# Kernel optimization log

Measured on AMD Instinct MI355X. Metric: run time of the kernel, lower is better.

## Reference

```python
import jax, jax.numpy as jnp
import numpy as np

B, L, D, H, HD, FF, NL = 2, 2048, 1024, 16, 64, 4096, 2
EPS = 1e-5
NEG = -1e30


def setup_inputs() -> dict:
    key = jax.random.key(0)
    ks = jax.random.split(key, 20)
    x = jax.random.normal(ks[0], (B, L, D), jnp.float32)
    # RoPE tables, rotate-half convention: [L, HD]
    pos = jnp.arange(L, dtype=jnp.float32)
    freqs = 1.0 / (10000.0 ** (jnp.arange(0, HD, 2, dtype=jnp.float32) / HD))
    ang = pos[:, None] * freqs[None, :]              # [L, HD/2]
    cos = jnp.concatenate([jnp.cos(ang), jnp.cos(ang)], -1)
    sin = jnp.concatenate([jnp.sin(ang), jnp.sin(ang)], -1)
    s = 0.02
    wq = jax.random.normal(ks[1], (NL, D, D), jnp.float32) * s
    wk = jax.random.normal(ks[2], (NL, D, D), jnp.float32) * s
    wv = jax.random.normal(ks[3], (NL, D, D), jnp.float32) * s
    wo = jax.random.normal(ks[4], (NL, D, D), jnp.float32) * s
    w1 = jax.random.normal(ks[5], (NL, D, FF), jnp.float32) * s
    w2 = jax.random.normal(ks[6], (NL, FF, D), jnp.float32) * s
    w3 = jax.random.normal(ks[7], (NL, D, FF), jnp.float32) * s
    attn_norm = jnp.ones((NL, D), jnp.float32)
    mlp_norm = jnp.ones((NL, D), jnp.float32)
    final_norm = jnp.ones((D,), jnp.float32)
    rw1 = jax.random.normal(ks[8], (D, D), jnp.float32) * s
    rb1 = jnp.zeros((D,), jnp.float32)
    rw2 = jax.random.normal(ks[9], (D, 1), jnp.float32) * s
    rb2 = jnp.zeros((1,), jnp.float32)
    return dict(x=x, cos=cos, sin=sin, wq=wq, wk=wk, wv=wv, wo=wo,
                w1=w1, w2=w2, w3=w3, attn_norm=attn_norm, mlp_norm=mlp_norm,
                final_norm=final_norm, rw1=rw1, rb1=rb1, rw2=rw2, rb2=rb2)


def _rms(x, w):
    return x * jax.lax.rsqrt(jnp.mean(x * x, -1, keepdims=True) + EPS) * w


def _rope(t, cos, sin):
    # t: [B, L, H, HD]; cos/sin: [L, HD]
    t1, t2 = jnp.split(t, 2, axis=-1)
    rot = jnp.concatenate([-t2, t1], -1)
    return t * cos[None, :, None, :] + rot * sin[None, :, None, :]


def reference(x, cos, sin, wq, wk, wv, wo, w1, w2, w3,
              attn_norm, mlp_norm, final_norm, rw1, rb1, rw2, rb2):
    causal = jnp.tril(jnp.ones((L, L), bool))
    h = x
    for i in range(NL):  # small fixed layer loop
        a = _rms(h, attn_norm[i])
        q = _rope((a @ wq[i]).reshape(B, L, H, HD), cos, sin)
        k = _rope((a @ wk[i]).reshape(B, L, H, HD), cos, sin)
        v = (a @ wv[i]).reshape(B, L, H, HD)
        sc = jnp.einsum('bqhd,bkhd->bhqk', q, k) / np.float32(np.sqrt(HD))
        sc = jnp.where(causal, sc, NEG)
        o = jnp.einsum('bhqk,bkhd->bqhd', jax.nn.softmax(sc, -1), v)
        h = h + o.reshape(B, L, D) @ wo[i]
        m = _rms(h, mlp_norm[i])
        h = h + (jax.nn.silu(m @ w1[i]) * (m @ w3[i])) @ w2[i]
    h = _rms(h, final_norm)

    # router chunking: straight-through hard boundaries
    logits = (jax.nn.silu(h @ rw1 + rb1) @ rw2 + rb2)[..., 0]   # [B, L]
    probs = jax.nn.sigmoid(logits)
    hard = (probs > 0.5).astype(h.dtype)
    mask = probs + jax.lax.stop_gradient(hard - probs)
    mask = mask.at[:, 0].set(1.0)
    mhard = jax.lax.stop_gradient(mask)
    # select matrix: S padded to static upper bound L (rows >= counts are zero)
    cums = jnp.cumsum(mhard, -1)                                # [B, L]
    seg = jnp.arange(1, L + 1, dtype=cums.dtype)[None, :, None] # [1, S, 1]
    assignment = (cums[:, None, :] == seg).astype(h.dtype)      # [B, S, L]
    select = assignment * mask[:, None, :]
    compressed = jnp.einsum('bsl,bld->bsd', select, h)          # [B, S, D]
    boundary_positions = jnp.argsort(-mhard, axis=-1)           # stable in jax
    counts = mhard.sum(-1).astype(jnp.int32)
    avg_chunk_size = jnp.float32(L) / jnp.mean(counts.astype(jnp.float32))
    return (h, compressed, boundary_positions, counts, avg_chunk_size)
```

## Files before the change

kernel.cpp:

```cpp
#include <hip/hip_runtime.h>
#include <cmath>

#define B_  2
#define L_  2048
#define D_  1024
#define H_  16
#define FF_ 4096
#define NL_ 2
#define NT_ (B_*L_)
#define ND_ (NT_*D_)

typedef __attribute__((ext_vector_type(8))) short bf16x8;
typedef __attribute__((ext_vector_type(4))) float f32x4;

__device__ __forceinline__ short f2bf(float x){
  unsigned u = __builtin_bit_cast(unsigned, x);
  unsigned r = (u + 0x7fffu + ((u>>16)&1u)) >> 16;
  return (short)r;
}
__device__ __forceinline__ float bf2f(short s){
  unsigned u = ((unsigned)(unsigned short)s) << 16;
  return __builtin_bit_cast(float, u);
}
#define MFMA16(a,b,c) __builtin_amdgcn_mfma_f32_16x16x32_bf16(a,b,c,0,0,0)

__device__ __forceinline__ void gload16(const short* g, short* l){
  __builtin_amdgcn_global_load_lds((const __attribute__((address_space(1))) void*)g,
                                   (__attribute__((address_space(3))) void*)l, 16, 0, 0);
}

template<bool WF32>
__global__ __launch_bounds__(256) void k_rmsnorm_s(const float* __restrict__ in,
                                                   const float* __restrict__ w,
                                                   short* __restrict__ oh,
                                                   short* __restrict__ ol,
                                                   float* __restrict__ of){
  int row = blockIdx.x; int tid = threadIdx.x;
  float4 xv = ((const float4*)(in + (size_t)row*D_))[tid];
  float ss = xv.x*xv.x + xv.y*xv.y + xv.z*xv.z + xv.w*xv.w;
  #pragma unroll
  for (int off=32; off; off>>=1) ss += __shfl_xor(ss, off);
  __shared__ float wsum[4];
  if ((tid&63)==0) wsum[tid>>6] = ss;
  __syncthreads();
  float tot = wsum[0]+wsum[1]+wsum[2]+wsum[3];
  float scale = 1.0f / sqrtf(tot*(1.0f/(float)D_) + 1e-5f);
  float4 w4 = ((const float4*)w)[tid];
  float v[4] = {xv.x*scale*w4.x, xv.y*scale*w4.y, xv.z*scale*w4.z, xv.w*scale*w4.w};
  short4 hh, ll;
  short h0=f2bf(v[0]); hh.x=h0; ll.x=f2bf(v[0]-bf2f(h0));
  short h1=f2bf(v[1]); hh.y=h1; ll.y=f2bf(v[1]-bf2f(h1));
  short h2=f2bf(v[2]); hh.z=h2; ll.z=f2bf(v[2]-bf2f(h2));
  short h3=f2bf(v[3]); hh.w=h3; ll.w=f2bf(v[3]-bf2f(h3));
  *(short4*)(oh + (size_t)row*D_ + tid*4) = hh;
  *(short4*)(ol + (size_t)row*D_ + tid*4) = ll;
  if (WF32){
    float4 ov; ov.x=v[0]; ov.y=v[1]; ov.z=v[2]; ov.w=v[3];
    ((float4*)(of + (size_t)row*D_))[tid] = ov;
  }
}

__global__ __launch_bounds__(256) void k_wsplit(const float* __restrict__ src,
                                                short* __restrict__ dh,
                                                short* __restrict__ dl,
                                                int srcN, int kOff, int nOff, int KT){
  __shared__ float t[64][68];
  int k0 = blockIdx.x*64, n0v = blockIdx.y*64;
  int tid = threadIdx.x;
  #pragma unroll
  for (int p=0;p<4;p++){
    int r = p*16 + (tid>>4);
    int c4 = (tid&15)*4;
    float4 v = *(const float4*)(src + (size_t)(kOff + k0 + r)*srcN + nOff + n0v + c4);
    *(float4*)&t[r][c4] = v;
  }
  __syncthreads();
  int n = tid>>2, kk = (tid&3)*16;
  bf16x8 H0, L0, H1, L1;
  #pragma unroll
  for (int q=0;q<8;q++){
    float v = t[kk+q][n]; short h=f2bf(v); H0[q]=h; L0[q]=f2bf(v-bf2f(h));
  }
  #pragma unroll
  for (int q=0;q<8;q++){
    float v = t[kk+8+q][n]; short h=f2bf(v); H1[q]=h; L1[q]=f2bf(v-bf2f(h));
  }
  size_t dof = (size_t)(n0v + n)*KT + k0 + kk;
  *(bf16x8*)(dh + dof) = H0;  *(bf16x8*)(dh + dof + 8) = H1;
  *(bf16x8*)(dl + dof) = L0;  *(bf16x8*)(dl + dof + 8) = L1;
}

__global__ __launch_bounds__(256,2) void k_qkv_mm(const short* __restrict__ Ah,
                                                  const short* __restrict__ Al,
                                                  const short* __restrict__ Wh,
                                                  const short* __restrict__ Wl,
                                                  short* __restrict__ OutH){
  __shared__ short lds[32768];
  int tid = threadIdx.x, wid = tid>>6, lane = tid&63;
  int l15 = lane&15, l4 = lane>>4;
  int wr = wid>>1, wc = wid&1;
  int m0 = blockIdx.y*128, n0 = blockIdx.x*128;
  const int K = 1024;
  f32x4 acc[4][4];
  #pragma unroll
  for (int i=0;i<4;i++){
    #pragma unroll
    for (int j=0;j<4;j++) acc[i][j] = (f32x4){0.f,0.f,0.f,0.f};
  }
  const short* gsrc = (wid==0)?Ah:(wid==1)?Al:(wid==2)?Wh:Wl;
  int rb = (wid<2)? m0 : n0;
  int gcol = ((lane&7)^(lane>>3))*8;
  short* ldsw = lds + wid*8192;
  const short* gp0 = gsrc + (size_t)(rb + (lane>>3))*K + gcol;
  for (int k0=0; k0<K; k0+=64){
    const short* gp = gp0 + k0;
    #pragma unroll
    for (int lc=0; lc<16; ++lc)
      gload16(gp + (size_t)lc*8*K, ldsw + lc*512);
    __syncthreads();
    #pragma unroll
    for (int ks=0; ks<2; ++ks){
      bf16x8 af[4], alf[4], wf[4], wlf[4];
      int gs = ((ks*4 + l4) ^ (lane&7))*8;
      #pragma unroll
      for (int f=0; f<4; ++f){
        int ar = (wr*64 + f*16 + l15)*64 + gs;
        af[f]  = *(const bf16x8*)&lds[ar];
        alf[f] = *(const bf16x8*)&lds[8192 + ar];
        int wr2 = (wc*64 + f*16 + l15)*64 + gs;
        wf[f]  = *(const bf16x8*)&lds[16384 + wr2];
        wlf[f] = *(const bf16x8*)&lds[24576 + wr2];
      }
      #pragma unroll
      for (int i=0;i<4;i++){
        #pragma unroll
        for (int j=0;j<4;j++){
          acc[i][j] = MFMA16(af[i],  wf[j],  acc[i][j]);
          acc[i][j] = MFMA16(alf[i], wf[j],  acc[i][j]);
          acc[i][j] = MFMA16(af[i],  wlf[j], acc[i][j]);
        }
      }
    }
    __syncthreads();
  }
  int sel = n0 >> 10;
  short* oh = OutH + (size_t)sel*8388608;
  short* ol = oh + 4194304;
  int cb = (n0 & 1023) + wc*64;
  #pragma unroll
  for (int i=0;i<4;i++){
    #pragma unroll
    for (int j=0;j<4;j++){
      #pragma unroll
      for (int r=0;r<4;r++){
        size_t mg = (size_t)(m0 + wr*64 + i*16 + l4*4 + r);
        int ng = cb + j*16 + l15;
        float v = acc[i][j][r];
        short h = f2bf(v);
        oh[mg*1024 + ng] = h;
        ol[mg*1024 + ng] = f2bf(v - bf2f(h));
      }
    }
  }
}

template<int EPI>
__global__ __launch_bounds__(256,2) void k_mm64(const short* __restrict__ Ah,
                                                const short* __restrict__ Al,
                                                const short* __restrict__ Wh,
                                                const short* __restrict__ Wl,
                                                const short* __restrict__ W3h,
                                                const short* __restrict__ W3l,
                                                int K,
                                                float* __restrict__ Cf,
                                                const float* __restrict__ bias,
                                                short* __restrict__ Gh,
                                                short* __restrict__ Gl,
                                                int ldc){
  __shared__ short lds[(EPI==3)?32768:24576];
  int tid = threadIdx.x, wid = tid>>6, lane = tid&63;
  int l15 = lane&15, l4 = lane>>4;
  int m0 = blockIdx.y*128, n0 = blockIdx.x*64;
  f32x4 a1[2][4], a3[2][4];
  #pragma unroll
  for (int i=0;i<2;i++){
    #pragma unroll
    for (int j=0;j<4;j++){ a1[i][j]=(f32x4){0.f,0.f,0.f,0.f}; a3[i][j]=(f32x4){0.f,0.f,0.f,0.f}; }
  }
  int gcol = ((lane&7)^(lane>>3))*8;
  int l8 = lane>>3;
  const int NCH = (EPI==3)? 16 : 12;
  for (int k0=0; k0<K; k0+=64){
    for (int t=0; t<NCH; ++t){
      int c = wid*NCH + t;
      const short* sb; int row0; short* db;
      if (c < 32){
        sb = (c<16)? Ah : Al; row0 = m0 + (c&15)*8;
        db = lds + ((c<16)?0:8192) + (c&15)*512;
      } else {
        int wseg = (c-32)>>3;
        sb = (wseg==0)?Wh:(wseg==1)?Wl:(wseg==2)?W3h:W3l;
        row0 = n0 + (c&7)*8;
        db = lds + 16384 + wseg*4096 + (c&7)*512;
      }
      gload16(sb + (size_t)(row0 + l8)*K + k0 + gcol, db);
    }
    __syncthreads();
    #pragma unroll
    for (int ks=0; ks<2; ++ks){
      int gs = ((ks*4 + l4) ^ (lane&7))*8;
      bf16x8 af[2], alf[2], wh[4], wl[4];
      #pragma unroll
      for (int f=0; f<2; ++f){
        int ar = (wid*32 + f*16 + l15)*64 + gs;
        af[f]  = *(const bf16x8*)&lds[ar];
        alf[f] = *(const bf16x8*)&lds[8192 + ar];
      }
      #pragma unroll
      for (int f=0; f<4; ++f){
        int wr2 = (f*16 + l15)*64 + gs;
        wh[f] = *(const bf16x8*)&lds[16384 + wr2];
        wl[f] = *(const bf16x8*)&lds[20480 + wr2];
      }
      #pragma unroll
      for (int i=0;i<2;i++){
        #pragma unroll
        for (int j=0;j<4;j++){
          a1[i][j] = MFMA16(af[i],  wh[j], a1[i][j]);
          a1[i][j] = MFMA16(alf[i], wh[j], a1[i][j]);
          a1[i][j] = MFMA16(af[i],  wl[j], a1[i][j]);
        }
      }
      if (EPI==3){
        bf16x8 w3h[4], w3l[4];
        #pragma unroll
        for (int f=0; f<4; ++f){
          int wr2 = (f*16 + l15)*64 + gs;
          w3h[f] = *(const bf16x8*)&lds[24576 + wr2];
          w3l[f] = *(const bf16x8*)&lds[28672 + wr2];
        }
        #pragma unroll
        for (int i=0;i<2;i++){
          #pragma unroll
          for (int j=0;j<4;j++){
            a3[i][j] = MFMA16(af[i],  w3h[j], a3[i][j]);
            a3[i][j] = MFMA16(alf[i], w3h[j], a3[i][j]);
            a3[i][j] = MFMA16(af[i],  w3l[j], a3[i][j]);
          }
        }
      }
    }
    __syncthreads();
  }
  #pragma unroll
  for (int i=0;i<2;i++){
    #pragma unroll
    for (int j=0;j<4;j++){
      #pragma unroll
      for (int r=0;r<4;r++){
        size_t mg = (size_t)(m0 + wid*32 + i*16 + l4*4 + r);
        int ng = n0 + j*16 + l15;
        float v = a1[i][j][r];
        if (EPI==1){
          float* cp = Cf + mg*ldc + ng;
          *cp = *cp + v;
        } else if (EPI==2){
          float x = v + bias[ng];
          Cf[mg*ldc + ng] = x/(1.f+expf(-x));
        } else {
          float g = v/(1.f+expf(-v)) * a3[i][j][r];
          short h = f2bf(g);
          Gh[mg*2048 + ng] = h;
          Gl[mg*2048 + ng] = f2bf(g - bf2f(h));
        }
      }
    }
  }
}

__global__ __launch_bounds__(256) void k_prep_k(const short* __restrict__ kh,
                                                const short* __restrict__ kl,
                                                const float* __restrict__ cosT,
                                                const float* __restrict__ sinT,
                                                short* __restrict__ kf){
  int wave = threadIdx.x>>6, lane = threadIdx.x&63;
  int t16 = blockIdx.x*4 + wave;
  int bh = blockIdx.y; int b = bh>>4, h = bh&15;
  int l15 = lane&15, l4 = lane>>4;
  int tok = t16*16 + l15;
  const short* khp = kh + (size_t)(b*L_+tok)*D_ + h*64;
  const short* klp = kl + (size_t)(b*L_+tok)*D_ + h*64;
  int d0 = l4*8;
  bf16x8 ka  = *(const bf16x8*)(khp + d0);
  bf16x8 kb2 = *(const bf16x8*)(khp + 32 + d0);
  bf16x8 kla = *(const bf16x8*)(klp + d0);
  bf16x8 klb = *(const bf16x8*)(klp + 32 + d0);
  const float* cr = cosT + (size_t)tok*64;
  const float* sr = sinT + (size_t)tok*64;
  float c0[8], s0[8], c1[8], s1[8];
  *(float4*)&c0[0] = *(const float4*)(cr + d0);      *(float4*)&c0[4] = *(const float4*)(cr + d0 + 4);
  *(float4*)&c1[0] = *(const float4*)(cr + 32 + d0); *(float4*)&c1[4] = *(const float4*)(cr + 32 + d0 + 4);
  *(float4*)&s0[0] = *(const float4*)(sr + d0);      *(float4*)&s0[4] = *(const float4*)(sr + d0 + 4);
  *(float4*)&s1[0] = *(const float4*)(sr + 32 + d0); *(float4*)&s1[4] = *(const float4*)(sr + 32 + d0 + 4);
  bf16x8 h0, lo0, h1, lo1;
  #pragma unroll
  for (int j=0;j<8;j++){
    float k0v = bf2f(ka[j]) + bf2f(kla[j]);
    float k1v = bf2f(kb2[j]) + bf2f(klb[j]);
    float r0 = k0v*c0[j] - k1v*s0[j];
    float r1 = k1v*c1[j] + k0v*s1[j];
    short a = f2bf(r0); h0[j]=a; lo0[j]=f2bf(r0 - bf2f(a));
    short bS = f2bf(r1); h1[j]=bS; lo1[j]=f2bf(r1 - bf2f(bS));
  }
  size_t base = ((size_t)(bh*128 + t16)*4)*512 + lane*8;
  *(bf16x8*)(kf + base)        = h0;
  *(bf16x8*)(kf + base + 512)  = lo0;
  *(bf16x8*)(kf + base + 1024) = h1;
  *(bf16x8*)(kf + base + 1536) = lo1;
}

__global__ __launch_bounds__(256) void k_prep_v(const short* __restrict__ vh,
                                                const short* __restrict__ vl,
                                                short* __restrict__ vf){
  int wave = threadIdx.x>>6, lane = threadIdx.x&63;
  int kc = blockIdx.x;
  int bh = blockIdx.y; int b = bh>>4, h = bh&15;
  int dt = wave;
  int l15 = lane&15, l4 = lane>>4;
  bf16x8 hi, lo;
  #pragma unroll
  for (int i=0;i<8;i++){
    size_t off = (size_t)(b*L_ + kc*32 + l4*8 + i)*D_ + h*64 + dt*16 + l15;
    hi[i] = vh[off];
    lo[i] = vl[off];
  }
  size_t base = (((size_t)(bh*64 + kc)*4 + dt)*2)*512 + lane*8;
  *(bf16x8*)(vf + base)       = hi;
  *(bf16x8*)(vf + base + 512) = lo;
}

__global__ __launch_bounds__(256) void k_attn_mfma(const short* __restrict__ qhb,
                                                   const short* __restrict__ qlb,
                                                   const short* __restrict__ kf,
                                                   const short* __restrict__ vf,
                                                   const float* __restrict__ cosT,
                                                   const float* __restrict__ sinT,
                                                   short* __restrict__ oh,
                                                   short* __restrict__ ol){
  int qt = 31 - (int)blockIdx.x;
  int bh = blockIdx.y; int b = bh>>4, h = bh&15;
  int wave = threadIdx.x>>6, lane = threadIdx.x&63;
  int l15 = lane&15, l4 = lane>>4;
  __shared__ short pblob[4][2048];
  short* pb = pblob[wave];

  int tok = qt*64 + wave*16 + l15;
  const short* qhp = qhb + (size_t)(b*L_+tok)*D_ + h*64;
  const short* qlp = qlb + (size_t)(b*L_+tok)*D_ + h*64;
  int d0 = l4*8;
  bf16x8 qa  = *(const bf16x8*)(qhp + d0);
  bf16x8 qb2 = *(const bf16x8*)(qhp + 32 + d0);
  bf16x8 qla = *(const bf16x8*)(qlp + d0);
  bf16x8 qlb2= *(const bf16x8*)(qlp + 32 + d0);
  const float* cr = cosT + (size_t)tok*64;
  const float* sr = sinT + (size_t)tok*64;
  float c0[8], s0[8], c1[8], s1[8];
  *(float4*)&c0[0] = *(const float4*)(cr + d0);      *(float4*)&c0[4] = *(const float4*)(cr + d0 + 4);
  *(float4*)&c1[0] = *(const float4*)(cr + 32 + d0); *(float4*)&c1[4] = *(const float4*)(cr + 32 + d0 + 4);
  *(float4*)&s0[0] = *(const float4*)(sr + d0);      *(float4*)&s0[4] = *(const float4*)(sr + d0 + 4);
  *(float4*)&s1[0] = *(const float4*)(sr + 32 + d0); *(float4*)&s1[4] = *(const float4*)(sr + 32 + d0 + 4);
  bf16x8 qh0, ql0, qh1, ql1;
  #pragma unroll
  for (int j=0;j<8;j++){
    float q0v = bf2f(qa[j]) + bf2f(qla[j]);
    float q1v = bf2f(qb2[j]) + bf2f(qlb2[j]);
    float r0 = (q0v*c0[j] - q1v*s0[j]) * 0.125f;
    float r1 = (q1v*c1[j] + q0v*s1[j]) * 0.125f;
    short a = f2bf(r0); qh0[j]=a; ql0[j]=f2bf(r0 - bf2f(a));
    short bS = f2bf(r1); qh1[j]=bS; ql1[j]=f2bf(r1 - bf2f(bS));
  }

  f32x4 O[4];
  #pragma unroll
  for (int dt=0;dt<4;dt++) O[dt] = (f32x4){0.f,0.f,0.f,0.f};
  float m_[4] = {-1e30f,-1e30f,-1e30f,-1e30f};
  float ls[4] = {0.f,0.f,0.f,0.f};

  for (int kt=0; kt<=qt; ++kt){
    bool dtile = (kt == qt);
    f32x4 sr4[4];
    const short* kbase = kf + ((size_t)(bh*128 + kt*4)*4)*512 + lane*8;
    #pragma unroll
    for (int g=0; g<4; g++){
      f32x4 acc = (f32x4){0.f,0.f,0.f,0.f};
      if (!(dtile && g > wave)){
        const short* kp = kbase + (size_t)g*2048;
        bf16x8 kh0 = *(const bf16x8*)(kp);
        bf16x8 kl0 = *(const bf16x8*)(kp + 512);
        bf16x8 kh1 = *(const bf16x8*)(kp + 1024);
        bf16x8 kl1 = *(const bf16x8*)(kp + 1536);
        acc = MFMA16(qh0, kh0, acc); acc = MFMA16(qh1, kh1, acc);
        acc = MFMA16(ql0, kh0, acc); acc = MFMA16(ql1, kh1, acc);
        acc = MFMA16(qh0, kl0, acc); acc = MFMA16(qh1, kl1, acc);
      }
      sr4[g] = acc;
    }
    float p_[4][4];
    #pragma unroll
    for (int r=0; r<4; r++){
      int rowrel = wave*16 + l4*4 + r;
      float mx = -1e30f;
      float sv[4];
      #pragma unroll
      for (int g=0; g<4; g++){
        float v = sr4[g][r];
        if (dtile && (g*16 + l15) > rowrel) v = -1e30f;
        sv[g] = v; mx = fmaxf(mx, v);
      }
      #pragma unroll
      for (int off=1; off<16; off<<=1) mx = fmaxf(mx, __shfl_xor(mx, off));
      float nm = fmaxf(m_[r], mx);
      float al = __expf(m_[r] - nm);
      m_[r] = nm;
      float ps = 0.f;
      #pragma unroll
      for (int g=0; g<4; g++){ float pv = __expf(sv[g] - nm); p_[g][r] = pv; ps += pv; }
      #pragma unroll
      for (int off=1; off<16; off<<=1) ps += __shfl_xor(ps, off);
      ls[r] = ls[r]*al + ps;
      #pragma unroll
      for (int dt=0; dt<4; dt++) O[dt][r] *= al;
    }
    #pragma unroll
    for (int g=0; g<4; g++){
      int key = g*16 + l15;
      int cc = key>>5, sub = (key>>3)&3, ii = key&7;
      #pragma unroll
      for (int r=0; r<4; r++){
        float pv = p_[g][r];
        short ph = f2bf(pv);
        short pl = f2bf(pv - bf2f(ph));
        int idx = cc*1024 + (sub*16 + l4*4 + r)*8 + ii;
        pb[idx] = ph;
        pb[idx + 512] = pl;
      }
    }
    asm volatile("s_waitcnt lgkmcnt(0)" ::: "memory");
    const short* vbase = vf + ((size_t)(bh*64 + kt*2)*8)*512 + lane*8;
    #pragma unroll
    for (int cc=0; cc<2; cc++){
      bf16x8 pah = *(const bf16x8*)(pb + cc*1024 + lane*8);
      bf16x8 pal = *(const bf16x8*)(pb + cc*1024 + 512 + lane*8);
      #pragma unroll
      for (int dt=0; dt<4; dt++){
        const short* vp = vbase + (size_t)cc*4096 + dt*1024;
        bf16x8 vh = *(const bf16x8*)(vp);
        bf16x8 vl = *(const bf16x8*)(vp + 512);
        O[dt] = MFMA16(pah, vh, O[dt]);
        O[dt] = MFMA16(pal, vh, O[dt]);
        O[dt] = MFMA16(pah, vl, O[dt]);
      }
    }
  }
  #pragma unroll
  for (int r=0; r<4; r++){
    float inv = 1.0f / ls[r];
    size_t row = (size_t)(b*L_ + qt*64 + wave*16 + l4*4 + r);
    #pragma unroll
    for (int dt=0; dt<4; dt++){
      float v = O[dt][r]*inv;
      short hh = f2bf(v);
      oh[row*D_ + h*64 + dt*16 + l15] = hh;
      ol[row*D_ + h*64 + dt*16 + l15] = f2bf(v - bf2f(hh));
    }
  }
}

__global__ __launch_bounds__(256) void k_gemv(const float* __restrict__ T,
                                              const float* __restrict__ rw2,
                                              const float* __restrict__ rb2,
                                              float* __restrict__ logits){
  int row = blockIdx.x; int tid = threadIdx.x;
  float4 tv = ((const float4*)(T + (size_t)row*D_))[tid];
  float4 wv = ((const float4*)rw2)[tid];
  float s = tv.x*wv.x + tv.y*wv.y + tv.z*wv.z + tv.w*wv.w;
  #pragma unroll
  for (int off=32; off; off>>=1) s += __shfl_xor(s, off);
  __shared__ float ps[4];
  if ((tid&63)==0) ps[tid>>6] = s;
  __syncthreads();
  if (tid==0) logits[row] = ps[0]+ps[1]+ps[2]+ps[3] + rb2[0];
}

__global__ __launch_bounds__(256) void k_boundary(const float* __restrict__ logits,
                                                  float* __restrict__ pos_out,
                                                  int* __restrict__ hard,
                                                  int* __restrict__ cums,
                                                  int* __restrict__ counts){
  int b = blockIdx.x; int tid = threadIdx.x;
  __shared__ int part[256];
  int loc[8]; int s=0;
  int base = b*L_;
  #pragma unroll
  for (int j=0;j<8;j++){
    int ll = tid*8 + j;
    float lg = logits[base+ll];
    int hv = (ll==0) ? 1 : ((lg > 0.0f) ? 1 : 0);
    loc[j]=hv; s+=hv;
  }
  part[tid]=s; __syncthreads();
  for (int off=1; off<256; off<<=1){
    int v = part[tid];
    int add = (tid>=off) ? part[tid-off] : 0;
    __syncthreads();
    part[tid] = v + add;
    __syncthreads();
  }
  int total = part[255];
  int run = part[tid] - s;
  #pragma unroll
  for (int j=0;j<8;j++){
    int ll = tid*8+j;
    run += loc[j];
    hard[base+ll] = loc[j];
    cums[base+ll] = run;
    int idx = loc[j] ? (run-1) : (total + ll - run);
    pos_out[base+idx] = (float)ll;
  }
  if (tid==0) counts[b] = total;
}

__global__ __launch_bounds__(256) void k_scatter(const float* __restrict__ hf,
                                                 const int* __restrict__ hard,
                                                 const int* __restrict__ cums,
                                                 float* __restrict__ comp){
  int rowid = blockIdx.x;
  if (!hard[rowid]) return;
  int b = rowid >> 11;
  int s = cums[rowid]-1;
  const float4* src = (const float4*)(hf + (size_t)rowid*D_);
  float4* dst = (float4*)(comp + (size_t)(b*L_ + s)*D_);
  dst[threadIdx.x] = src[threadIdx.x];
}

__global__ void k_finalize(const int* __restrict__ counts, float* __restrict__ out){
  if (threadIdx.x==0 && blockIdx.x==0){
    float c0 = (float)counts[0], c1 = (float)counts[1];
    out[0]=c0; out[1]=c1;
    out[2] = (float)L_ / (0.5f*(c0+c1));
  }
}

extern "C" void kernel_launch(void* const* d_in, const int* in_sizes, int n_in,
                              void* d_out, int out_size, void* d_ws, size_t ws_size,
                              hipStream_t stream){
  const float* x      = (const float*)d_in[0];
  const float* cosT   = (const float*)d_in[1];
  const float* sinT   = (const float*)d_in[2];
  const float* wq     = (const float*)d_in[3];
  const float* wk     = (const float*)d_in[4];
  const float* wv     = (const float*)d_in[5];
  const float* wo     = (const float*)d_in[6];
  const float* w1     = (const float*)d_in[7];
  const float* w2     = (const float*)d_in[8];
  const float* w3     = (const float*)d_in[9];
  const float* attn_n = (const float*)d_in[10];
  const float* mlp_n  = (const float*)d_in[11];
  const float* final_n= (const float*)d_in[12];
  const float* rw1    = (const float*)d_in[13];
  const float* rb1    = (const float*)d_in[14];
  const float* rw2    = (const float*)d_in[15];
  const float* rb2    = (const float*)d_in[16];

  float* outF = (float*)d_out;
  float* hD   = outF;
  float* compD= outF + (size_t)ND_;
  float* posD = outF + (size_t)2*ND_;

  char* WS = (char*)d_ws;
  auto S = [&](size_t mb){ return (short*)(WS + mb*1048576ull); };
  auto F = [&](size_t mb){ return (float*)(WS + mb*1048576ull); };
  short *ah=S(0), *al=S(8);
  short *qh=S(16), *ql=S(24), *kh=S(32), *kl=S(40), *vh=S(48), *vl=S(56);
  short *qkvwt_h=S(64), *qkvwt_l=S(70);
  short *vf=S(64);
  short *kf=S(48);
  short *wot_h=S(32), *wot_l=S(34);
  short *gh=S(16), *gl=S(32);
  short *w1t_h=S(48), *w1t_l=S(52), *w3t_h=S(56), *w3t_l=S(60);
  short *w2t_h=S(64), *w2t_l=S(68);
  short *rw1t_h=S(16), *rw1t_l=S(18);
  float *ra=F(20);
  float *logits=F(76);
  int *hard=(int*)(logits+NT_), *cums=hard+NT_, *cnts=cums+NT_;
  short *oh=(short*)compD, *ol=oh+4194304;

  hipMemcpyAsync(hD, x, (size_t)ND_*sizeof(float), hipMemcpyDeviceToDevice, stream);

  for (int i=0;i<NL_;++i){
    k_rmsnorm_s<false><<<NT_,256,0,stream>>>(hD, attn_n + (size_t)i*D_, ah, al, nullptr);
    k_wsplit<<<dim3(16,16),256,0,stream>>>(wq + (size_t)i*D_*D_, qkvwt_h,         qkvwt_l,         1024, 0, 0, 1024);
    k_wsplit<<<dim3(16,16),256,0,stream>>>(wk + (size_t)i*D_*D_, qkvwt_h+1048576, qkvwt_l+1048576, 1024, 0, 0, 1024);
    k_wsplit<<<dim3(16,16),256,0,stream>>>(wv + (size_t)i*D_*D_, qkvwt_h+2097152, qkvwt_l+2097152, 1024, 0, 0, 1024);
    k_qkv_mm<<<dim3(24,32),256,0,stream>>>(ah, al, qkvwt_h, qkvwt_l, qh);
    k_prep_v<<<dim3(64,32),256,0,stream>>>(vh, vl, vf);
    k_prep_k<<<dim3(32,32),256,0,stream>>>(kh, kl, cosT, sinT, kf);
    k_wsplit<<<dim3(16,16),256,0,stream>>>(wo + (size_t)i*D_*D_, wot_h, wot_l, 1024, 0, 0, 1024);
    k_attn_mfma<<<dim3(32,32),256,0,stream>>>(qh, ql, kf, vf, cosT, sinT, oh, ol);
    k_mm64<1><<<dim3(16,32),256,0,stream>>>(oh, ol, wot_h, wot_l, nullptr, nullptr,
                                            1024, hD, nullptr, nullptr, nullptr, 1024);
    k_rmsnorm_s<false><<<NT_,256,0,stream>>>(hD, mlp_n + (size_t)i*D_, ah, al, nullptr);
    for (int hc=0; hc<2; ++hc){
      k_wsplit<<<dim3(16,32),256,0,stream>>>(w1 + (size_t)i*D_*FF_, w1t_h, w1t_l, 4096, 0, hc*2048, 1024);
      k_wsplit<<<dim3(16,32),256,0,stream>>>(w3 + (size_t)i*D_*FF_, w3t_h, w3t_l, 4096, 0, hc*2048, 1024);
      k_wsplit<<<dim3(32,16),256,0,stream>>>(w2 + (size_t)i*FF_*D_, w2t_h, w2t_l, 1024, hc*2048, 0, 2048);
      k_mm64<3><<<dim3(32,32),256,0,stream>>>(ah, al, w1t_h, w1t_l, w3t_h, w3t_l,
                                              1024, nullptr, nullptr, gh, gl, 0);
      k_mm64<1><<<dim3(16,32),256,0,stream>>>(gh, gl, w2t_h, w2t_l, nullptr, nullptr,
                                              2048, hD, nullptr, nullptr, nullptr, 1024);
    }
  }
  k_rmsnorm_s<true><<<NT_,256,0,stream>>>(hD, final_n, ah, al, hD);
  k_wsplit<<<dim3(16,16),256,0,stream>>>(rw1, rw1t_h, rw1t_l, 1024, 0, 0, 1024);
  k_mm64<2><<<dim3(16,32),256,0,stream>>>(ah, al, rw1t_h, rw1t_l, nullptr, nullptr,
                                          1024, ra, rb1, nullptr, nullptr, 1024);
  k_gemv<<<NT_,256,0,stream>>>(ra, rw2, rb2, logits);
  k_boundary<<<B_,256,0,stream>>>(logits, posD, hard, cums, cnts);
  hipMemsetAsync(compD, 0, (size_t)ND_*sizeof(float), stream);
  k_scatter<<<NT_,256,0,stream>>>(hD, hard, cums, compD);
  k_finalize<<<1,64,0,stream>>>(cnts, posD + NT_);
}
```

Before: 1.494 ms.

## Pipeline attention K/V through LDS, pair causal tiles, swizzle GEMM blocks across XCDs

The attention kernel now stages K and V tiles into double-buffered LDS with async global-to-LDS loads that overlap compute. Each block handles a complementary pair of causal query tiles to balance work, and blocks are remapped across XCDs. The GEMM kernels get an XCD-aware block swizzle for L2 locality and s_setprio around MFMA bursts, and non-gated k_mm64 variants get a higher occupancy hint. The cost is extra LDS and barriers in attention, possible register pressure from the occupancy change, and fewer but longer attention blocks.

```diff
diff --git a/kernel.cpp b/kernel.cpp
--- a/kernel.cpp
+++ b/kernel.cpp
@@ -27,6 +27,14 @@
 __device__ __forceinline__ void gload16(const short* g, short* l){
   __builtin_amdgcn_global_load_lds((const __attribute__((address_space(1))) void*)g,
                                    (__attribute__((address_space(3))) void*)l, 16, 0, 0);
+}
+
+__device__ __forceinline__ int2 xcd_swizzle(){
+  int gx = gridDim.x;
+  int n  = gx * gridDim.y;
+  int hw = blockIdx.x + gx*blockIdx.y;
+  int logical = (hw&7)*(n>>3) + (hw>>3);
+  return make_int2(logical % gx, logical / gx);
 }
 
 template<bool WF32>
@@ -99,7 +107,8 @@
   int tid = threadIdx.x, wid = tid>>6, lane = tid&63;
   int l15 = lane&15, l4 = lane>>4;
   int wr = wid>>1, wc = wid&1;
-  int m0 = blockIdx.y*128, n0 = blockIdx.x*128;
+  int2 bxy = xcd_swizzle();
+  int m0 = bxy.y*128, n0 = bxy.x*128;
   const int K = 1024;
   f32x4 acc[4][4];
   #pragma unroll
@@ -131,6 +140,7 @@
         wf[f]  = *(const bf16x8*)&lds[16384 + wr2];
         wlf[f] = *(const bf16x8*)&lds[24576 + wr2];
       }
+      __builtin_amdgcn_s_setprio(1);
       #pragma unroll
       for (int i=0;i<4;i++){
         #pragma unroll
@@ -140,6 +150,7 @@
           acc[i][j] = MFMA16(af[i],  wlf[j], acc[i][j]);
         }
       }
+      __builtin_amdgcn_s_setprio(0);
     }
     __syncthreads();
   }
@@ -165,7 +176,7 @@
 }
 
 template<int EPI>
-__global__ __launch_bounds__(256,2) void k_mm64(const short* __restrict__ Ah,
+__global__ __launch_bounds__(256,(EPI==3)?2:3) void k_mm64(const short* __restrict__ Ah,
                                                 const short* __restrict__ Al,
                                                 const short* __restrict__ Wh,
                                                 const short* __restrict__ Wl,
@@ -180,7 +191,8 @@
   __shared__ short lds[(EPI==3)?32768:24576];
   int tid = threadIdx.x, wid = tid>>6, lane = tid&63;
   int l15 = lane&15, l4 = lane>>4;
-  int m0 = blockIdx.y*128, n0 = blockIdx.x*64;
+  int2 bxy = xcd_swizzle();
+  int m0 = bxy.y*128, n0 = bxy.x*64;
   f32x4 a1[2][4], a3[2][4];
   #pragma unroll
   for (int i=0;i<2;i++){
@@ -222,6 +234,7 @@
         wh[f] = *(const bf16x8*)&lds[16384 + wr2];
         wl[f] = *(const bf16x8*)&lds[20480 + wr2];
       }
+      __builtin_amdgcn_s_setprio(1);
       #pragma unroll
       for (int i=0;i<2;i++){
         #pragma unroll
@@ -231,6 +244,7 @@
           a1[i][j] = MFMA16(af[i],  wl[j], a1[i][j]);
         }
       }
+      __builtin_amdgcn_s_setprio(0);
       if (EPI==3){
         bf16x8 w3h[4], w3l[4];
         #pragma unroll
@@ -239,6 +253,7 @@
           w3h[f] = *(const bf16x8*)&lds[24576 + wr2];
           w3l[f] = *(const bf16x8*)&lds[28672 + wr2];
         }
+        __builtin_amdgcn_s_setprio(1);
         #pragma unroll
         for (int i=0;i<2;i++){
           #pragma unroll
@@ -248,6 +263,7 @@
             a3[i][j] = MFMA16(af[i],  w3l[j], a3[i][j]);
           }
         }
+        __builtin_amdgcn_s_setprio(0);
       }
     }
     __syncthreads();
@@ -347,131 +363,165 @@
                                                    const float* __restrict__ sinT,
                                                    short* __restrict__ oh,
                                                    short* __restrict__ ol){
-  int qt = 31 - (int)blockIdx.x;
-  int bh = blockIdx.y; int b = bh>>4, h = bh&15;
+  int bid = blockIdx.x;
+  int logical = (bid&7)*64 + (bid>>3);
+  int bh = logical>>4, pair = logical&15;
+  int b = bh>>4, h = bh&15;
   int wave = threadIdx.x>>6, lane = threadIdx.x&63;
   int l15 = lane&15, l4 = lane>>4;
+  __shared__ short kvs[2][16384];
   __shared__ short pblob[4][2048];
   short* pb = pblob[wave];
 
-  int tok = qt*64 + wave*16 + l15;
-  const short* qhp = qhb + (size_t)(b*L_+tok)*D_ + h*64;
-  const short* qlp = qlb + (size_t)(b*L_+tok)*D_ + h*64;
-  int d0 = l4*8;
-  bf16x8 qa  = *(const bf16x8*)(qhp + d0);
-  bf16x8 qb2 = *(const bf16x8*)(qhp + 32 + d0);
-  bf16x8 qla = *(const bf16x8*)(qlp + d0);
-  bf16x8 qlb2= *(const bf16x8*)(qlp + 32 + d0);
-  const float* cr = cosT + (size_t)tok*64;
-  const float* sr = sinT + (size_t)tok*64;
-  float c0[8], s0[8], c1[8], s1[8];
-  *(float4*)&c0[0] = *(const float4*)(cr + d0);      *(float4*)&c0[4] = *(const float4*)(cr + d0 + 4);
-  *(float4*)&c1[0] = *(const float4*)(cr + 32 + d0); *(float4*)&c1[4] = *(const float4*)(cr + 32 + d0 + 4);
-  *(float4*)&s0[0] = *(const float4*)(sr + d0);      *(float4*)&s0[4] = *(const float4*)(sr + d0 + 4);
-  *(float4*)&s1[0] = *(const float4*)(sr + 32 + d0); *(float4*)&s1[4] = *(const float4*)(sr + 32 + d0 + 4);
-  bf16x8 qh0, ql0, qh1, ql1;
-  #pragma unroll
-  for (int j=0;j<8;j++){
-    float q0v = bf2f(qa[j]) + bf2f(qla[j]);
-    float q1v = bf2f(qb2[j]) + bf2f(qlb2[j]);
-    float r0 = (q0v*c0[j] - q1v*s0[j]) * 0.125f;
-    float r1 = (q1v*c1[j] + q0v*s1[j]) * 0.125f;
-    short a = f2bf(r0); qh0[j]=a; ql0[j]=f2bf(r0 - bf2f(a));
-    short bS = f2bf(r1); qh1[j]=bS; ql1[j]=f2bf(r1 - bf2f(bS));
-  }
-
-  f32x4 O[4];
-  #pragma unroll
-  for (int dt=0;dt<4;dt++) O[dt] = (f32x4){0.f,0.f,0.f,0.f};
-  float m_[4] = {-1e30f,-1e30f,-1e30f,-1e30f};
-  float ls[4] = {0.f,0.f,0.f,0.f};
-
-  for (int kt=0; kt<=qt; ++kt){
-    bool dtile = (kt == qt);
-    f32x4 sr4[4];
-    const short* kbase = kf + ((size_t)(bh*128 + kt*4)*4)*512 + lane*8;
-    #pragma unroll
-    for (int g=0; g<4; g++){
-      f32x4 acc = (f32x4){0.f,0.f,0.f,0.f};
-      if (!(dtile && g > wave)){
-        const short* kp = kbase + (size_t)g*2048;
-        bf16x8 kh0 = *(const bf16x8*)(kp);
-        bf16x8 kl0 = *(const bf16x8*)(kp + 512);
-        bf16x8 kh1 = *(const bf16x8*)(kp + 1024);
-        bf16x8 kl1 = *(const bf16x8*)(kp + 1536);
-        acc = MFMA16(qh0, kh0, acc); acc = MFMA16(qh1, kh1, acc);
-        acc = MFMA16(ql0, kh0, acc); acc = MFMA16(ql1, kh1, acc);
-        acc = MFMA16(qh0, kl0, acc); acc = MFMA16(qh1, kl1, acc);
-      }
-      sr4[g] = acc;
-    }
-    float p_[4][4];
+  auto stage = [&](int bufi, int kt){
+    const short* kg = kf + ((size_t)(bh*128 + kt*4))*2048;
+    const short* vg = vf + ((size_t)(bh*64 + kt*2))*4096;
+    short* dst = kvs[bufi];
+    #pragma unroll
+    for (int c=0;c<8;c++){
+      int ch = wave*8 + c;
+      const short* src = (ch<16)? (kg + ch*512) : (vg + (ch-16)*512);
+      gload16(src + lane*8, dst + ch*512);
+    }
+  };
+
+  for (int half=0; half<2; ++half){
+    int qt = (half==0) ? (31-pair) : pair;
+    stage(0, 0);
+    int tok = qt*64 + wave*16 + l15;
+    const short* qhp = qhb + (size_t)(b*L_+tok)*D_ + h*64;
+    const short* qlp = qlb + (size_t)(b*L_+tok)*D_ + h*64;
+    int d0 = l4*8;
+    bf16x8 qa  = *(const bf16x8*)(qhp + d0);
+    bf16x8 qb2 = *(const bf16x8*)(qhp + 32 + d0);
+    bf16x8 qla = *(const bf16x8*)(qlp + d0);
+    bf16x8 qlb2= *(const bf16x8*)(qlp + 32 + d0);
+    const float* cr = cosT + (size_t)tok*64;
+    const float* sr = sinT + (size_t)tok*64;
+    float c0[8], s0[8], c1[8], s1[8];
+    *(float4*)&c0[0] = *(const float4*)(cr + d0);      *(float4*)&c0[4] = *(const float4*)(cr + d0 + 4);
+    *(float4*)&c1[0] = *(const float4*)(cr + 32 + d0); *(float4*)&c1[4] = *(const float4*)(cr + 32 + d0 + 4);
+    *(float4*)&s0[0] = *(const float4*)(sr + d0);      *(float4*)&s0[4] = *(const float4*)(sr + d0 + 4);
+    *(float4*)&s1[0] = *(const float4*)(sr + 32 + d0); *(float4*)&s1[4] = *(const float4*)(sr + 32 + d0 + 4);
+    bf16x8 qh0, ql0, qh1, ql1;
+    #pragma unroll
+    for (int j=0;j<8;j++){
+      float q0v = bf2f(qa[j]) + bf2f(qla[j]);
+      float q1v = bf2f(qb2[j]) + bf2f(qlb2[j]);
+      float r0 = (q0v*c0[j] - q1v*s0[j]) * 0.125f;
+      float r1 = (q1v*c1[j] + q0v*s1[j]) * 0.125f;
+      short a = f2bf(r0); qh0[j]=a; ql0[j]=f2bf(r0 - bf2f(a));
+      short bS = f2bf(r1); qh1[j]=bS; ql1[j]=f2bf(r1 - bf2f(bS));
+    }
+
+    f32x4 O[4];
+    #pragma unroll
+    for (int dt=0;dt<4;dt++) O[dt] = (f32x4){0.f,0.f,0.f,0.f};
+    float m_[4] = {-1e30f,-1e30f,-1e30f,-1e30f};
+    float ls[4] = {0.f,0.f,0.f,0.f};
+
+    int cur = 0;
+    for (int kt=0; kt<=qt; ++kt){
+      bool haveNext = (kt < qt);
+      if (haveNext){
+        stage(cur^1, kt+1);
+        asm volatile("s_waitcnt vmcnt(8)" ::: "memory");
+      } else {
+        asm volatile("s_waitcnt vmcnt(0)" ::: "memory");
+      }
+      __builtin_amdgcn_s_barrier();
+      const short* Kl = kvs[cur];
+      const short* Vl = kvs[cur] + 8192;
+      bool dtile = (kt == qt);
+      f32x4 sr4[4];
+      #pragma unroll
+      for (int g=0; g<4; g++){
+        f32x4 acc = (f32x4){0.f,0.f,0.f,0.f};
+        if (!(dtile && g > wave)){
+          const short* kp = Kl + g*2048 + lane*8;
+          bf16x8 kh0 = *(const bf16x8*)(kp);
+          bf16x8 kl0 = *(const bf16x8*)(kp + 512);
+          bf16x8 kh1 = *(const bf16x8*)(kp + 1024);
+          bf16x8 kl1 = *(const bf16x8*)(kp + 1536);
+          __builtin_amdgcn_s_setprio(1);
+          acc = MFMA16(qh0, kh0, acc); acc = MFMA16(qh1, kh1, acc);
+          acc = MFMA16(ql0, kh0, acc); acc = MFMA16(ql1, kh1, acc);
+          acc = MFMA16(qh0, kl0, acc); acc = MFMA16(qh1, kl1, acc);
+          __builtin_amdgcn_s_setprio(0);
+        }
+        sr4[g] = acc;
+      }
+      float p_[4][4];
+      #pragma unroll
+      for (int r=0; r<4; r++){
+        int rowrel = wave*16 + l4*4 + r;
+        float mx = -1e30f;
+        float sv[4];
+        #pragma unroll
+        for (int g=0; g<4; g++){
+          float v = sr4[g][r];
+          if (dtile && (g*16 + l15) > rowrel) v = -1e30f;
+          sv[g] = v; mx = fmaxf(mx, v);
+        }
+        #pragma unroll
+        for (int off=1; off<16; off<<=1) mx = fmaxf(mx, __shfl_xor(mx, off));
+        float nm = fmaxf(m_[r], mx);
+        float al = __expf(m_[r] - nm);
+        m_[r] = nm;
+        float ps = 0.f;
+        #pragma unroll
+        for (int g=0; g<4; g++){ float pv = __expf(sv[g] - nm); p_[g][r] = pv; ps += pv; }
+        #pragma unroll
+        for (int off=1; off<16; off<<=1) ps += __shfl_xor(ps, off);
+        ls[r] = ls[r]*al + ps;
+        #pragma unroll
+        for (int dt=0; dt<4; dt++) O[dt][r] *= al;
+      }
+      #pragma unroll
+      for (int g=0; g<4; g++){
+        int key = g*16 + l15;
+        int cc = key>>5, sub = (key>>3)&3, ii = key&7;
+        #pragma unroll
+        for (int r=0; r<4; r++){
+          float pv = p_[g][r];
+          short ph = f2bf(pv);
+          short pl = f2bf(pv - bf2f(ph));
+          int idx = cc*1024 + (sub*16 + l4*4 + r)*8 + ii;
+          pb[idx] = ph;
+          pb[idx + 512] = pl;
+        }
+      }
+      asm volatile("s_waitcnt lgkmcnt(0)" ::: "memory");
+      #pragma unroll
+      for (int cc=0; cc<2; cc++){
+        bf16x8 pah = *(const bf16x8*)(pb + cc*1024 + lane*8);
+        bf16x8 pal = *(const bf16x8*)(pb + cc*1024 + 512 + lane*8);
+        const short* vp = Vl + cc*4096 + lane*8;
+        __builtin_amdgcn_s_setprio(1);
+        #pragma unroll
+        for (int dt=0; dt<4; dt++){
+          bf16x8 vh = *(const bf16x8*)(vp + dt*1024);
+          bf16x8 vl = *(const bf16x8*)(vp + dt*1024 + 512);
+          O[dt] = MFMA16(pah, vh, O[dt]);
+          O[dt] = MFMA16(pal, vh, O[dt]);
+          O[dt] = MFMA16(pah, vl, O[dt]);
+        }
+        __builtin_amdgcn_s_setprio(0);
+      }
+      __builtin_amdgcn_s_barrier();
+      cur ^= 1;
+    }
     #pragma unroll
     for (int r=0; r<4; r++){
-      int rowrel = wave*16 + l4*4 + r;
-      float mx = -1e30f;
-      float sv[4];
-      #pragma unroll
-      for (int g=0; g<4; g++){
-        float v = sr4[g][r];
-        if (dtile && (g*16 + l15) > rowrel) v = -1e30f;
-        sv[g] = v; mx = fmaxf(mx, v);
-      }
-      #pragma unroll
-      for (int off=1; off<16; off<<=1) mx = fmaxf(mx, __shfl_xor(mx, off));
-      float nm = fmaxf(m_[r], mx);
-      float al = __expf(m_[r] - nm);
-      m_[r] = nm;
-      float ps = 0.f;
-      #pragma unroll
-      for (int g=0; g<4; g++){ float pv = __expf(sv[g] - nm); p_[g][r] = pv; ps += pv; }
-      #pragma unroll
-      for (int off=1; off<16; off<<=1) ps += __shfl_xor(ps, off);
-      ls[r] = ls[r]*al + ps;
-      #pragma unroll
-      for (int dt=0; dt<4; dt++) O[dt][r] *= al;
-    }
-    #pragma unroll
-    for (int g=0; g<4; g++){
-      int key = g*16 + l15;
-      int cc = key>>5, sub = (key>>3)&3, ii = key&7;
-      #pragma unroll
-      for (int r=0; r<4; r++){
-        float pv = p_[g][r];
-        short ph = f2bf(pv);
-        short pl = f2bf(pv - bf2f(ph));
-        int idx = cc*1024 + (sub*16 + l4*4 + r)*8 + ii;
-        pb[idx] = ph;
-        pb[idx + 512] = pl;
-      }
-    }
-    asm volatile("s_waitcnt lgkmcnt(0)" ::: "memory");
-    const short* vbase = vf + ((size_t)(bh*64 + kt*2)*8)*512 + lane*8;
-    #pragma unroll
-    for (int cc=0; cc<2; cc++){
-      bf16x8 pah = *(const bf16x8*)(pb + cc*1024 + lane*8);
-      bf16x8 pal = *(const bf16x8*)(pb + cc*1024 + 512 + lane*8);
+      float inv = 1.0f / ls[r];
+      size_t row = (size_t)(b*L_ + qt*64 + wave*16 + l4*4 + r);
       #pragma unroll
       for (int dt=0; dt<4; dt++){
-        const short* vp = vbase + (size_t)cc*4096 + dt*1024;
-        bf16x8 vh = *(const bf16x8*)(vp);
-        bf16x8 vl = *(const bf16x8*)(vp + 512);
-        O[dt] = MFMA16(pah, vh, O[dt]);
-        O[dt] = MFMA16(pal, vh, O[dt]);
-        O[dt] = MFMA16(pah, vl, O[dt]);
-      }
-    }
-  }
-  #pragma unroll
-  for (int r=0; r<4; r++){
-    float inv = 1.0f / ls[r];
-    size_t row = (size_t)(b*L_ + qt*64 + wave*16 + l4*4 + r);
-    #pragma unroll
-    for (int dt=0; dt<4; dt++){
-      float v = O[dt][r]*inv;
-      short hh = f2bf(v);
-      oh[row*D_ + h*64 + dt*16 + l15] = hh;
-      ol[row*D_ + h*64 + dt*16 + l15] = f2bf(v - bf2f(hh));
+        float v = O[dt][r]*inv;
+        short hh = f2bf(v);
+        oh[row*D_ + h*64 + dt*16 + l15] = hh;
+        ol[row*D_ + h*64 + dt*16 + l15] = f2bf(v - bf2f(hh));
+      }
     }
   }
 }
@@ -606,7 +656,7 @@
     k_prep_v<<<dim3(64,32),256,0,stream>>>(vh, vl, vf);
     k_prep_k<<<dim3(32,32),256,0,stream>>>(kh, kl, cosT, sinT, kf);
     k_wsplit<<<dim3(16,16),256,0,stream>>>(wo + (size_t)i*D_*D_, wot_h, wot_l, 1024, 0, 0, 1024);
-    k_attn_mfma<<<dim3(32,32),256,0,stream>>>(qh, ql, kf, vf, cosT, sinT, oh, ol);
+    k_attn_mfma<<<dim3(512),256,0,stream>>>(qh, ql, kf, vf, cosT, sinT, oh, ol);
     k_mm64<1><<<dim3(16,32),256,0,stream>>>(oh, ol, wot_h, wot_l, nullptr, nullptr,
                                             1024, hD, nullptr, nullptr, nullptr, 1024);
     k_rmsnorm_s<false><<<NT_,256,0,stream>>>(hD, mlp_n + (size_t)i*D_, ah, al, nullptr);
```

Result: faster. 1.256 ms (-15.9%).
